# Performance work log

Hardware: AMD Instinct MI355X
Metric: run time of the kernel (lower is better)

Reference implementation:

```python
import jax, jax.numpy as jnp
import numpy as np

B, P, K = 32, 2048, 20   # events, points per event, kNN neighbors
EPS = 1e-5               # BatchNorm eps (eval mode, running stats)


def setup_inputs() -> dict:
    key = jax.random.key(0)
    ks = iter(jax.random.split(key, 64))
    inp = {}
    inp["x"] = jax.random.normal(next(ks), (B * P, 7), jnp.float32)
    inp["batch"] = jnp.repeat(jnp.arange(B, dtype=jnp.int32), P)

    def add_layer(tag, cin, cout):
        inp["w" + tag] = jax.random.normal(next(ks), (cin, cout), jnp.float32) / np.sqrt(cin)
        inp["b" + tag] = jax.random.normal(next(ks), (cout,), jnp.float32) * 0.01
        inp["g" + tag] = jax.random.uniform(next(ks), (cout,), jnp.float32, 0.5, 1.5)
        inp["e" + tag] = jax.random.normal(next(ks), (cout,), jnp.float32) * 0.1
        inp["m" + tag] = jax.random.normal(next(ks), (cout,), jnp.float32) * 0.1
        inp["v" + tag] = jax.random.uniform(next(ks), (cout,), jnp.float32, 0.5, 1.5)

    # conv1 MLP: [14, 64, 64, 64]
    add_layer("10", 14, 64)
    add_layer("11", 64, 64)
    add_layer("12", 64, 64)
    # conv2 MLP: [128, 128]
    add_layer("20", 128, 128)
    return inp


def _lin_relu_bn(h, W, b, g, be, rm, rv):
    # Linear -> ReLU -> BatchNorm1d (eval mode: running stats)
    h = jax.nn.relu(h @ W + b)
    return (h - rm) * (g / jnp.sqrt(rv + EPS)) + be


def _knn_idx(x):
    # x: [B, P, C] -> indices of K nearest neighbors (incl. self), [B, P, K]
    sq = jnp.sum(x * x, axis=-1)                                   # [B, P]
    d = sq[:, :, None] + sq[:, None, :] - 2.0 * jnp.einsum("bpc,bqc->bpq", x, x)
    _, idx = jax.lax.top_k(-d, K)
    return idx


def _edge_conv(x, mlp):
    # DynamicEdgeConv: kNN graph on current features, edge MLP([x_i, x_j - x_i]), max-aggr
    idx = _knn_idx(x)                                              # [B, P, K]
    xj = jax.vmap(lambda xb, ib: xb[ib])(x, idx)                   # [B, P, K, C]
    xi = jnp.broadcast_to(x[:, :, None, :], xj.shape)
    e = jnp.concatenate([xi, xj - xi], axis=-1)                    # [B, P, K, 2C]
    return jnp.max(mlp(e), axis=2)                                 # [B, P, Cout]


def reference(x, batch,
              w10, b10, g10, e10, m10, v10,
              w11, b11, g11, e11, m11, v11,
              w12, b12, g12, e12, m12, v12,
              w20, b20, g20, e20, m20, v20):
    xb = x.reshape(B, P, -1)                                       # fixed-size events

    def mlp1(e):
        h = _lin_relu_bn(e, w10, b10, g10, e10, m10, v10)
        h = _lin_relu_bn(h, w11, b11, g11, e11, m11, v11)
        return _lin_relu_bn(h, w12, b12, g12, e12, m12, v12)

    def mlp2(e):
        return _lin_relu_bn(e, w20, b20, g20, e20, m20, v20)

    x1 = _edge_conv(xb, mlp1)                                      # [B, P, 64]
    x2 = _edge_conv(x1, mlp2)                                      # [B, P, 128]
    out = jnp.concatenate([x1, x2], axis=-1).reshape(B * P, 192)
    return out, batch
```

## Files before the change

### kernel.cpp

```cpp
#include <hip/hip_runtime.h>

#define B_EV 32
#define P_PT 2048
#define K_NN 20
#define NPTS (B_EV*P_PT)
#define EPS_BN 1e-5f
#define RINF 3.0e38f

typedef _Float16 half8 __attribute__((ext_vector_type(8)));
typedef float f32x4 __attribute__((ext_vector_type(4)));

static constexpr int oWA10=0, oWB10=448, oB10=896, oT10=960,
  oT11=5184,
  oT12=9408,
  oWA20=9472, oWB20=17664, oB20=25856, oT20=25984,
  oB11p=26048, oB12p=26112,
  oW11hi=26176, oW11lo=28224,
  oW12hi=30272, oW12lo=32320;
static constexpr size_t oIDX = 36864;
static constexpr size_t oA1  = 1347584;
static constexpr size_t oB1  = oA1 + (size_t)NPTS*64;
static constexpr size_t oV2  = oB1 + (size_t)NPTS*64;
static constexpr size_t oX1  = oV2 + (size_t)NPTS*128;
static constexpr size_t oSQ  = oX1 + (size_t)NPTS*64;
static constexpr size_t oU2  = oA1;

__global__ __launch_bounds__(128) void k_prep(
  const float* w10,const float* b10,const float* g10,const float* e10,const float* m10,const float* v10,
  const float* w11,const float* b11,const float* g11,const float* e11,const float* m11,const float* v11,
  const float* w12,const float* b12,const float* g12,const float* e12,const float* m12,const float* v12,
  const float* w20,const float* b20,const float* g20,const float* e20,const float* m20,const float* v20,
  float* ws)
{
  __shared__ float t10s[64], t11s[64];
  int c = threadIdx.x;
  if (c < 64) {
    float s0 = g10[c]*rsqrtf(v10[c]+EPS_BN);
    ws[oB10+c]=b10[c]*s0;
    float t10 = e10[c]-m10[c]*s0; ws[oT10+c]=t10; t10s[c]=t10;
    for (int i=0;i<7;i++){
      ws[oWA10+i*64+c]=(w10[i*64+c]-w10[(7+i)*64+c])*s0;
      ws[oWB10+i*64+c]=w10[(7+i)*64+c]*s0;
    }
    float s1 = g11[c]*rsqrtf(v11[c]+EPS_BN);
    float t11 = e11[c]-m11[c]*s1; ws[oT11+c]=t11; t11s[c]=t11;
    float s2 = g12[c]*rsqrtf(v12[c]+EPS_BN);
    ws[oT12+c]=e12[c]-m12[c]*s2;
  }
  __syncthreads();
  if (c < 64) {
    float s1 = g11[c]*rsqrtf(v11[c]+EPS_BN);
    _Float16* W1hi = (_Float16*)(ws + oW11hi);
    _Float16* W1lo = (_Float16*)(ws + oW11lo);
    float acc = b11[c]*s1;
    for (int i=0;i<64;i++){
      float wv = w11[i*64+c]*s1;
      _Float16 h = (_Float16)wv;
      W1hi[c*64+i] = h;
      W1lo[c*64+i] = (_Float16)(wv - (float)h);
      acc = fmaf(t10s[i], wv, acc);
    }
    ws[oB11p+c]=acc;
    float s2 = g12[c]*rsqrtf(v12[c]+EPS_BN);
    _Float16* W2hi = (_Float16*)(ws + oW12hi);
    _Float16* W2lo = (_Float16*)(ws + oW12lo);
    float acc2 = b12[c]*s2;
    for (int i=0;i<64;i++){
      float wv = w12[i*64+c]*s2;
      _Float16 h = (_Float16)wv;
      W2hi[c*64+i] = h;
      W2lo[c*64+i] = (_Float16)(wv - (float)h);
      acc2 = fmaf(t11s[i], wv, acc2);
    }
    ws[oB12p+c]=acc2;
  }
  {
    float s = g20[c]*rsqrtf(v20[c]+EPS_BN);
    ws[oB20+c]=b20[c]*s; ws[oT20+c]=e20[c]-m20[c]*s;
    for (int i=0;i<64;i++){
      ws[oWA20+i*128+c]=(w20[i*128+c]-w20[(64+i)*128+c])*s;
      ws[oWB20+i*128+c]=w20[(64+i)*128+c]*s;
    }
  }
}

__device__ __forceinline__ void select20(float (&d)[32], int lane, int base, int g,
                                         int* __restrict__ idxout)
{
  float g4[4];
  #pragma unroll
  for (int k=0;k<4;k++){
    float m = d[8*k];
    #pragma unroll
    for (int j=1;j<8;j++) m = fminf(m, d[8*k+j]);
    g4[k]=m;
  }
  float T = 0.f;
  #pragma unroll 1
  for (int pass=0; pass<20; ++pass){
    float m = fminf(fminf(g4[0],g4[1]), fminf(g4[2],g4[3]));
    #pragma unroll
    for (int off=32; off>0; off>>=1) m = fminf(m, __shfl_xor(m, off, 64));
    if (pass==19){ T=m; break; }
    #pragma unroll
    for (int k=0;k<4;k++){
      if (g4[k]==m){
        #pragma unroll
        for (int j=0;j<8;j++) d[8*k+j] = (d[8*k+j]==m) ? RINF : d[8*k+j];
        float mm = d[8*k];
        #pragma unroll
        for (int j=1;j<8;j++) mm = fminf(mm, d[8*k+j]);
        g4[k]=mm;
      }
    }
  }
  int cnt=0;
  #pragma unroll
  for (int j=0;j<32;j++){
    bool take = (d[j]>=RINF) || (d[j]==T);
    unsigned long long mb = __ballot(take);
    if (take){
      int pos = cnt + (int)__popcll(mb & ((1ull<<lane)-1ull));
      if (pos < K_NN) idxout[(size_t)g*K_NN + pos] = base + j*64 + lane;
    }
    cnt += (int)__popcll(mb);
  }
  if (lane==0){
    for (int r=cnt; r<K_NN; ++r) idxout[(size_t)g*K_NN + r] = g;
  }
}

__global__ __launch_bounds__(1024, 8) void k_knn1(const float* __restrict__ x, int* __restrict__ idxout)
{
  __shared__ float xs[P_PT*8];
  int t = threadIdx.x;
  int b = blockIdx.x;
  int xcd = b & 7, kk = b >> 3;
  int e = xcd + ((kk >> 7) << 3);
  int blk = kk & 127;
  {
    const float* xe = x + (size_t)e*P_PT*7;
    #pragma unroll
    for (int u=0; u<2; u++){
      int p = t + u*1024;
      float v0=xe[p*7+0], v1=xe[p*7+1], v2=xe[p*7+2], v3=xe[p*7+3];
      float v4=xe[p*7+4], v5=xe[p*7+5], v6=xe[p*7+6];
      int s = (p&7)<<2;
      int w0 = (p*8) ^ s;
      int w1 = (p*8+4) ^ s;
      f32x4 lo = {v0,v1,v2,v3};
      f32x4 hi = {v4,v5,v6,0.f};
      *(f32x4*)(xs + w0) = lo;
      *(f32x4*)(xs + w1) = hi;
    }
  }
  __syncthreads();
  int lane = t & 63;
  int g = e*P_PT + blk*16 + (t>>6);
  int pin = g & (P_PT-1);
  float xp[7];
  {
    int s = (pin&7)<<2;
    f32x4 lo = *(const f32x4*)(xs + ((pin*8)^s));
    f32x4 hi = *(const f32x4*)(xs + ((pin*8+4)^s));
    xp[0]=lo[0]; xp[1]=lo[1]; xp[2]=lo[2]; xp[3]=lo[3];
    xp[4]=hi[0]; xp[5]=hi[1]; xp[6]=hi[2];
  }
  int sl = (lane&7)<<2;
  const float* base0 = xs + ((lane*8)^sl);
  const float* base1 = xs + ((lane*8+4)^sl);
  float d[32];
  #pragma unroll
  for (int j=0;j<32;j++){
    f32x4 lo = *(const f32x4*)(base0 + j*512);
    f32x4 hi = *(const f32x4*)(base1 + j*512);
    float s=0.f, df;
    df = xp[0]-lo[0]; s=fmaf(df,df,s);
    df = xp[1]-lo[1]; s=fmaf(df,df,s);
    df = xp[2]-lo[2]; s=fmaf(df,df,s);
    df = xp[3]-lo[3]; s=fmaf(df,df,s);
    df = xp[4]-hi[0]; s=fmaf(df,df,s);
    df = xp[5]-hi[1]; s=fmaf(df,df,s);
    df = xp[6]-hi[2]; s=fmaf(df,df,s);
    d[j]=s;
  }
  select20(d, lane, e*P_PT, g, idxout);
}

__global__ __launch_bounds__(256) void k_ab1(const float* __restrict__ x, const float* __restrict__ W,
                                             float* __restrict__ A1, float* __restrict__ B1)
{
  int g = blockIdx.x*256+threadIdx.x;
  float xi[7];
  #pragma unroll
  for (int i=0;i<7;i++) xi[i]=x[(size_t)g*7+i];
  float a[64], b[64];
  #pragma unroll
  for (int c=0;c<64;c++){ a[c]=W[oB10+c]; b[c]=0.f; }
  #pragma unroll
  for (int i=0;i<7;i++){
    #pragma unroll
    for (int c=0;c<64;c++) a[c]=fmaf(xi[i], W[oWA10+i*64+c], a[c]);
    #pragma unroll
    for (int c=0;c<64;c++) b[c]=fmaf(xi[i], W[oWB10+i*64+c], b[c]);
  }
  #pragma unroll
  for (int c=0;c<64;c+=4){
    float4 oa; oa.x=a[c]; oa.y=a[c+1]; oa.z=a[c+2]; oa.w=a[c+3];
    *(float4*)(A1+(size_t)g*64+c)=oa;
    float4 ob; ob.x=b[c]; ob.y=b[c+1]; ob.z=b[c+2]; ob.w=b[c+3];
    *(float4*)(B1+(size_t)g*64+c)=ob;
  }
}

__global__ __launch_bounds__(256, 2) void k_ec1m(const int* __restrict__ idx, const float* __restrict__ ws,
    const float* __restrict__ A1, const float* __restrict__ B1,
    float* __restrict__ x1, float* __restrict__ sqv, float* __restrict__ out)
{
  __shared__ float h2s[4][48*64];
  int t = threadIdx.x, w = t>>6, lane = t&63;
  int b = blockIdx.x;
  int xcd = b & 7, kk = b >> 3;
  int ev = xcd + ((kk >> 8) << 3);
  int iA = ev*P_PT + (kk & 255)*8 + w*2;
  int iB = iA + 1;
  int lg = lane>>4, lr = lane&15;

  int jT0 = idx[(size_t)iA*K_NN + lr];
  int jT1 = idx[(size_t)iB*K_NN + lr];
  int a2 = (lr < 4) ? iA*K_NN + 16 + lr : iB*K_NN + 12 + lr;
  a2 = (lr < 8) ? a2 : 0;
  int jT2 = (lr < 8) ? idx[a2] : iA;

  const float* ApA = A1 + (size_t)iA*64;
  const float* ApB = A1 + (size_t)iB*64;
  float4 avA[2][2], avB[2][2], bv[3][2][2];
  const float* Bp0 = B1 + (size_t)jT0*64;
  const float* Bp1 = B1 + (size_t)jT1*64;
  const float* Bp2 = B1 + (size_t)jT2*64;
  #pragma unroll
  for (int ks=0;ks<2;ks++){
    int c0 = ks*32 + lg*8;
    avA[ks][0] = *(const float4*)(ApA+c0); avA[ks][1] = *(const float4*)(ApA+c0+4);
    avB[ks][0] = *(const float4*)(ApB+c0); avB[ks][1] = *(const float4*)(ApB+c0+4);
    bv[0][ks][0] = *(const float4*)(Bp0+c0); bv[0][ks][1] = *(const float4*)(Bp0+c0+4);
    bv[1][ks][0] = *(const float4*)(Bp1+c0); bv[1][ks][1] = *(const float4*)(Bp1+c0+4);
    bv[2][ks][0] = *(const float4*)(Bp2+c0); bv[2][ks][1] = *(const float4*)(Bp2+c0+4);
  }

  bool useB2 = (lr >= 4) && (lr < 8);
  half8 AH[3][2], AL[3][2];
  #pragma unroll
  for (int tile=0;tile<3;tile++){
    #pragma unroll
    for (int ks=0;ks<2;ks++){
      float4 a0, a1;
      if (tile==0){ a0 = avA[ks][0]; a1 = avA[ks][1]; }
      else if (tile==1){ a0 = avB[ks][0]; a1 = avB[ks][1]; }
      else {
        a0.x = useB2 ? avB[ks][0].x : avA[ks][0].x;  a0.y = useB2 ? avB[ks][0].y : avA[ks][0].y;
        a0.z = useB2 ? avB[ks][0].z : avA[ks][0].z;  a0.w = useB2 ? avB[ks][0].w : avA[ks][0].w;
        a1.x = useB2 ? avB[ks][1].x : avA[ks][1].x;  a1.y = useB2 ? avB[ks][1].y : avA[ks][1].y;
        a1.z = useB2 ? avB[ks][1].z : avA[ks][1].z;  a1.w = useB2 ? avB[ks][1].w : avA[ks][1].w;
      }
      float hv[8];
      hv[0]=fmaxf(a0.x+bv[tile][ks][0].x,0.f); hv[1]=fmaxf(a0.y+bv[tile][ks][0].y,0.f);
      hv[2]=fmaxf(a0.z+bv[tile][ks][0].z,0.f); hv[3]=fmaxf(a0.w+bv[tile][ks][0].w,0.f);
      hv[4]=fmaxf(a1.x+bv[tile][ks][1].x,0.f); hv[5]=fmaxf(a1.y+bv[tile][ks][1].y,0.f);
      hv[6]=fmaxf(a1.z+bv[tile][ks][1].z,0.f); hv[7]=fmaxf(a1.w+bv[tile][ks][1].w,0.f);
      half8 ah, al;
      #pragma unroll
      for (int q=0;q<8;q++){
        _Float16 h = (_Float16)hv[q];
        ah[q]=h; al[q]=(_Float16)(hv[q]-(float)h);
      }
      AH[tile][ks]=ah; AL[tile][ks]=al;
    }
  }

  f32x4 acc[3][4];
  #pragma unroll
  for (int nt=0;nt<4;nt++){
    float bb = ws[oB11p + nt*16 + lr];
    f32x4 v = {bb,bb,bb,bb};
    acc[0][nt]=v; acc[1][nt]=v; acc[2][nt]=v;
  }
  {
    const _Float16* W1hi = (const _Float16*)(ws + oW11hi);
    const _Float16* W1lo = (const _Float16*)(ws + oW11lo);
    #pragma unroll
    for (int nt=0;nt<4;nt++){
      const _Float16* whp = W1hi + (nt*16+lr)*64 + lg*8;
      const _Float16* wlp = W1lo + (nt*16+lr)*64 + lg*8;
      half8 wh0 = *(const half8*)(whp);
      half8 wh1 = *(const half8*)(whp+32);
      half8 wl0 = *(const half8*)(wlp);
      half8 wl1 = *(const half8*)(wlp+32);
      #pragma unroll
      for (int tile=0;tile<3;tile++){
        acc[tile][nt] = __builtin_amdgcn_mfma_f32_16x16x32_f16(AH[tile][0], wh0, acc[tile][nt], 0,0,0);
        acc[tile][nt] = __builtin_amdgcn_mfma_f32_16x16x32_f16(AL[tile][0], wh0, acc[tile][nt], 0,0,0);
        acc[tile][nt] = __builtin_amdgcn_mfma_f32_16x16x32_f16(AH[tile][0], wl0, acc[tile][nt], 0,0,0);
        acc[tile][nt] = __builtin_amdgcn_mfma_f32_16x16x32_f16(AH[tile][1], wh1, acc[tile][nt], 0,0,0);
        acc[tile][nt] = __builtin_amdgcn_mfma_f32_16x16x32_f16(AL[tile][1], wh1, acc[tile][nt], 0,0,0);
        acc[tile][nt] = __builtin_amdgcn_mfma_f32_16x16x32_f16(AH[tile][1], wl1, acc[tile][nt], 0,0,0);
      }
    }
  }

  float* hb = h2s[w];
  #pragma unroll
  for (int tile=0;tile<3;tile++){
    #pragma unroll
    for (int nt=0;nt<4;nt++){
      #pragma unroll
      for (int r=0;r<4;r++){
        int row = tile*16 + lg*4 + r;
        int col = nt*16 + lr;
        int baddr = (row*256 + col*4) ^ ((row&7)<<4);
        *(float*)((char*)hb + baddr) = fmaxf(acc[tile][nt][r], 0.f);
      }
    }
  }

  half8 AH2[3][2], AL2[3][2];
  #pragma unroll
  for (int tile=0;tile<3;tile++){
    #pragma unroll
    for (int ks=0;ks<2;ks++){
      int row = tile*16 + lr;
      int byte0 = (row*256 + (ks*32 + lg*8)*4);
      int s = (row&7)<<4;
      f32x4 v0 = *(const f32x4*)((char*)hb + ((byte0)^s));
      f32x4 v1 = *(const f32x4*)((char*)hb + ((byte0+16)^s));
      half8 ah, al;
      #pragma unroll
      for (int q=0;q<4;q++){
        _Float16 h = (_Float16)v0[q];
        ah[q]=h; al[q]=(_Float16)(v0[q]-(float)h);
      }
      #pragma unroll
      for (int q=0;q<4;q++){
        _Float16 h = (_Float16)v1[q];
        ah[4+q]=h; al[4+q]=(_Float16)(v1[q]-(float)h);
      }
      AH2[tile][ks]=ah; AL2[tile][ks]=al;
    }
  }

  f32x4 acc2[3][4];
  #pragma unroll
  for (int nt=0;nt<4;nt++){
    float bb = ws[oB12p + nt*16 + lr];
    f32x4 v = {bb,bb,bb,bb};
    acc2[0][nt]=v; acc2[1][nt]=v; acc2[2][nt]=v;
  }
  {
    const _Float16* W2hi = (const _Float16*)(ws + oW12hi);
    const _Float16* W2lo = (const _Float16*)(ws + oW12lo);
    #pragma unroll
    for (int nt=0;nt<4;nt++){
      const _Float16* whp = W2hi + (nt*16+lr)*64 + lg*8;
      const _Float16* wlp = W2lo + (nt*16+lr)*64 + lg*8;
      half8 wh0 = *(const half8*)(whp);
      half8 wh1 = *(const half8*)(whp+32);
      half8 wl0 = *(const half8*)(wlp);
      half8 wl1 = *(const half8*)(wlp+32);
      #pragma unroll
      for (int tile=0;tile<3;tile++){
        acc2[tile][nt] = __builtin_amdgcn_mfma_f32_16x16x32_f16(AH2[tile][0], wh0, acc2[tile][nt], 0,0,0);
        acc2[tile][nt] = __builtin_amdgcn_mfma_f32_16x16x32_f16(AL2[tile][0], wh0, acc2[tile][nt], 0,0,0);
        acc2[tile][nt] = __builtin_amdgcn_mfma_f32_16x16x32_f16(AH2[tile][0], wl0, acc2[tile][nt], 0,0,0);
        acc2[tile][nt] = __builtin_amdgcn_mfma_f32_16x16x32_f16(AH2[tile][1], wh1, acc2[tile][nt], 0,0,0);
        acc2[tile][nt] = __builtin_amdgcn_mfma_f32_16x16x32_f16(AL2[tile][1], wh1, acc2[tile][nt], 0,0,0);
        acc2[tile][nt] = __builtin_amdgcn_mfma_f32_16x16x32_f16(AH2[tile][1], wl1, acc2[tile][nt], 0,0,0);
      }
    }
  }

  float finA[4], finB[4];
  float sqA = 0.f, sqB = 0.f;
  #pragma unroll
  for (int nt=0;nt<4;nt++){
    float cvA = -RINF;
    #pragma unroll
    for (int r=0;r<4;r++) cvA = fmaxf(cvA, acc2[0][nt][r]);
    if (lg==0){
      #pragma unroll
      for (int r=0;r<4;r++) cvA = fmaxf(cvA, acc2[2][nt][r]);
    }
    cvA = fmaxf(cvA, __shfl_xor(cvA,16,64));
    cvA = fmaxf(cvA, __shfl_xor(cvA,32,64));
    finA[nt] = fmaxf(cvA, 0.f) + ws[oT12 + nt*16 + lr];
    sqA = fmaf(finA[nt], finA[nt], sqA);

    float cvB = -RINF;
    #pragma unroll
    for (int r=0;r<4;r++) cvB = fmaxf(cvB, acc2[1][nt][r]);
    if (lg==1){
      #pragma unroll
      for (int r=0;r<4;r++) cvB = fmaxf(cvB, acc2[2][nt][r]);
    }
    cvB = fmaxf(cvB, __shfl_xor(cvB,16,64));
    cvB = fmaxf(cvB, __shfl_xor(cvB,32,64));
    finB[nt] = fmaxf(cvB, 0.f) + ws[oT12 + nt*16 + lr];
    sqB = fmaf(finB[nt], finB[nt], sqB);
  }
  if (lane < 16){
    #pragma unroll
    for (int nt=0;nt<4;nt++){
      x1[(size_t)iA*64 + nt*16 + lane] = finA[nt];
      out[(size_t)iA*192 + nt*16 + lane] = finA[nt];
      x1[(size_t)iB*64 + nt*16 + lane] = finB[nt];
      out[(size_t)iB*192 + nt*16 + lane] = finB[nt];
    }
  }
  #pragma unroll
  for (int off=1; off<16; off<<=1){
    sqA += __shfl_xor(sqA, off, 64);
    sqB += __shfl_xor(sqB, off, 64);
  }
  if (lane == 0){ sqv[iA] = sqA; sqv[iB] = sqB; }
}

__global__ __launch_bounds__(1024, 4) void k_dsel(const float* __restrict__ x1,
    const float* __restrict__ sqv, int* __restrict__ idxout)
{
  __shared__ float cs[16][260];
  int t = threadIdx.x, w = t>>6, lane = t&63;
  int b = blockIdx.x;
  int xcd = b & 7, kk = b >> 3;
  int e = xcd + ((kk >> 7) << 3);
  int base16 = e*P_PT + (kk & 127)*16;
  int lg = lane>>4, lr = lane&15;

  half8 AH[2], AL[2];
  {
    const float* Ap = x1 + (size_t)(base16 + lr)*64;
    #pragma unroll
    for (int kx=0;kx<2;kx++){
      float4 a0 = *(const float4*)(Ap + kx*32 + lg*8);
      float4 a1 = *(const float4*)(Ap + kx*32 + lg*8 + 4);
      float hv[8] = {a0.x,a0.y,a0.z,a0.w,a1.x,a1.y,a1.z,a1.w};
      half8 ah, al;
      #pragma unroll
      for (int q=0;q<8;q++){
        _Float16 h = (_Float16)hv[q];
        ah[q]=h; al[q]=(_Float16)(hv[q]-(float)h);
      }
      AH[kx]=ah; AL[kx]=al;
    }
  }
  int p = base16 + w;
  float sqp = sqv[p];
  const float* Xe = x1 + (size_t)e*P_PT*64;
  const float* sqe = sqv + e*P_PT;

  float d[32];
  #pragma unroll 1
  for (int chunk=0; chunk<8; ++chunk){
    int c = chunk*256 + w*16 + lr;
    const float* Bp = Xe + (size_t)c*64;
    f32x4 acc = {0.f,0.f,0.f,0.f};
    #pragma unroll
    for (int kx=0;kx<2;kx++){
      float4 b0 = *(const float4*)(Bp + kx*32 + lg*8);
      float4 b1 = *(const float4*)(Bp + kx*32 + lg*8 + 4);
      float hv[8] = {b0.x,b0.y,b0.z,b0.w,b1.x,b1.y,b1.z,b1.w};
      half8 bh, bl;
      #pragma unroll
      for (int q=0;q<8;q++){
        _Float16 h = (_Float16)hv[q];
        bh[q]=h; bl[q]=(_Float16)(hv[q]-(float)h);
      }
      acc = __builtin_amdgcn_mfma_f32_16x16x32_f16(AH[kx], bh, acc, 0,0,0);
      acc = __builtin_amdgcn_mfma_f32_16x16x32_f16(AL[kx], bh, acc, 0,0,0);
      acc = __builtin_amdgcn_mfma_f32_16x16x32_f16(AH[kx], bl, acc, 0,0,0);
      acc = __builtin_amdgcn_mfma_f32_16x16x32_f16(AL[kx], bl, acc, 0,0,0);
    }
    #pragma unroll
    for (int r=0;r<4;r++) cs[4*lg + r][w*16 + lr] = acc[r];
    __syncthreads();
    #pragma unroll
    for (int jj=0;jj<4;jj++){
      float sqc = sqe[chunk*256 + jj*64 + lane];
      d[chunk*4 + jj] = sqp + sqc - 2.f*cs[w][jj*64 + lane];
    }
    __syncthreads();
  }
  select20(d, lane, e*P_PT, p, idxout);
}

__global__ __launch_bounds__(256) void k_uv2(const float* __restrict__ x1, const float* __restrict__ W,
                                             float* __restrict__ U2, float* __restrict__ V2)
{
  int g = blockIdx.x*256 + threadIdx.x;
  int half = blockIdx.y & 1;
  bool isU = blockIdx.y < 2;
  const float* Wb = W + (isU?oWA20:oWB20) + half*64;
  float acc[64];
  #pragma unroll
  for (int c=0;c<64;c++) acc[c] = isU ? W[oB20+half*64+c] : 0.f;
  const float* xp = x1 + (size_t)g*64;
  #pragma unroll 1
  for (int i=0;i<64;i+=4){
    float4 xv = *(const float4*)(xp+i);
    #pragma unroll
    for (int c=0;c<64;c++) acc[c]=fmaf(xv.x, Wb[(i+0)*128+c], acc[c]);
    #pragma unroll
    for (int c=0;c<64;c++) acc[c]=fmaf(xv.y, Wb[(i+1)*128+c], acc[c]);
    #pragma unroll
    for (int c=0;c<64;c++) acc[c]=fmaf(xv.z, Wb[(i+2)*128+c], acc[c]);
    #pragma unroll
    for (int c=0;c<64;c++) acc[c]=fmaf(xv.w, Wb[(i+3)*128+c], acc[c]);
  }
  float* dst = (isU?U2:V2) + (size_t)g*128 + half*64;
  #pragma unroll
  for (int c=0;c<64;c+=4){
    float4 o; o.x=acc[c]; o.y=acc[c+1]; o.z=acc[c+2]; o.w=acc[c+3];
    *(float4*)(dst+c)=o;
  }
}

__global__ __launch_bounds__(256) void k_gather2(const int* __restrict__ idx, const float* __restrict__ U2,
     const float* __restrict__ V2, const float* __restrict__ W, const int* __restrict__ batch,
     float* __restrict__ out)
{
  int b = blockIdx.x;
  int xcd = b & 7, kk = b >> 3;
  int ev = xcd + ((kk >> 3) << 3);
  int g = ev*P_PT + (kk & 7)*256 + threadIdx.x;
  int half = blockIdx.y;
  if (half == 0) out[(size_t)NPTS*192 + g] = (float)batch[g];
  float mx[64];
  #pragma unroll
  for (int c=0;c<64;c++) mx[c]=-RINF;
  for (int k=0;k<K_NN;k++){
    int j = idx[(size_t)g*K_NN+k];
    const float4* vp = (const float4*)(V2 + (size_t)j*128 + half*64);
    #pragma unroll
    for (int c4=0;c4<16;c4++){
      float4 v=vp[c4];
      mx[c4*4+0]=fmaxf(mx[c4*4+0],v.x);
      mx[c4*4+1]=fmaxf(mx[c4*4+1],v.y);
      mx[c4*4+2]=fmaxf(mx[c4*4+2],v.z);
      mx[c4*4+3]=fmaxf(mx[c4*4+3],v.w);
    }
  }
  const float* Up = U2 + (size_t)g*128 + half*64;
  float* op = out + (size_t)g*192 + 64 + half*64;
  #pragma unroll
  for (int c=0;c<64;c+=4){
    float4 o;
    o.x = fmaxf(Up[c+0]+mx[c+0],0.f)+W[oT20+half*64+c+0];
    o.y = fmaxf(Up[c+1]+mx[c+1],0.f)+W[oT20+half*64+c+1];
    o.z = fmaxf(Up[c+2]+mx[c+2],0.f)+W[oT20+half*64+c+2];
    o.w = fmaxf(Up[c+3]+mx[c+3],0.f)+W[oT20+half*64+c+3];
    *(float4*)(op+c)=o;
  }
}

extern "C" void kernel_launch(void* const* d_in, const int* in_sizes, int n_in,
                              void* d_out, int out_size, void* d_ws, size_t ws_size,
                              hipStream_t stream)
{
  const float* x     = (const float*)d_in[0];
  const int*   batch = (const int*)d_in[1];
  const float* w10=(const float*)d_in[2],  *b10=(const float*)d_in[3],  *g10=(const float*)d_in[4],
             *e10=(const float*)d_in[5],  *m10=(const float*)d_in[6],  *v10=(const float*)d_in[7];
  const float* w11=(const float*)d_in[8],  *b11=(const float*)d_in[9],  *g11=(const float*)d_in[10],
             *e11=(const float*)d_in[11], *m11=(const float*)d_in[12], *v11=(const float*)d_in[13];
  const float* w12=(const float*)d_in[14], *b12=(const float*)d_in[15], *g12=(const float*)d_in[16],
             *e12=(const float*)d_in[17], *m12=(const float*)d_in[18], *v12=(const float*)d_in[19];
  const float* w20=(const float*)d_in[20], *b20=(const float*)d_in[21], *g20=(const float*)d_in[22],
             *e20=(const float*)d_in[23], *m20=(const float*)d_in[24], *v20=(const float*)d_in[25];

  float* ws  = (float*)d_ws;
  float* out = (float*)d_out;
  int*   idxp = (int*)(ws + oIDX);

  k_prep<<<1,128,0,stream>>>(w10,b10,g10,e10,m10,v10, w11,b11,g11,e11,m11,v11,
                             w12,b12,g12,e12,m12,v12, w20,b20,g20,e20,m20,v20, ws);
  k_knn1<<<NPTS/16, 1024, 0, stream>>>(x, idxp);
  k_ab1<<<NPTS/256, 256, 0, stream>>>(x, ws, ws+oA1, ws+oB1);
  k_ec1m<<<NPTS/8, 256, 0, stream>>>(idxp, ws, ws+oA1, ws+oB1, ws+oX1, ws+oSQ, out);
  k_dsel<<<NPTS/16, 1024, 0, stream>>>(ws+oX1, ws+oSQ, idxp);
  k_uv2<<<dim3(NPTS/256,4),256,0,stream>>>(ws+oX1, ws, ws+oU2, ws+oV2);
  k_gather2<<<dim3(NPTS/256,2),256,0,stream>>>(idxp, ws+oU2, ws+oV2, ws, batch, out);
}
```

Measured before the change: 1.096 ms.

## Precompute fp16 hi/lo split of x1 in edge-conv kernel; halve dsel barriers

The edge-conv kernel now writes x1 a second time as two fp16 arrays, a high part and a residual low part, so the distance/select kernel loads half8 operands directly. This removes the fp32 loads and per-element conversion in the MFMA distance loop. The dsel loop also processes 512 candidates per shared-memory round instead of 256, which halves the number of __syncthreads and doubles the LDS buffer. The cost is extra global writes in k_ec1m, plus more shared memory per block, which could reduce occupancy.

```diff
diff --git a/kernel.cpp b/kernel.cpp
--- a/kernel.cpp
+++ b/kernel.cpp
@@ -23,6 +23,8 @@
 static constexpr size_t oV2  = oB1 + (size_t)NPTS*64;
 static constexpr size_t oX1  = oV2 + (size_t)NPTS*128;
 static constexpr size_t oSQ  = oX1 + (size_t)NPTS*64;
+static constexpr size_t oX1H = oSQ + (size_t)NPTS;
+static constexpr size_t oX1L = oX1H + (size_t)NPTS*32;
 static constexpr size_t oU2  = oA1;
 
 __global__ __launch_bounds__(128) void k_prep(
@@ -215,7 +217,8 @@
 
 __global__ __launch_bounds__(256, 2) void k_ec1m(const int* __restrict__ idx, const float* __restrict__ ws,
     const float* __restrict__ A1, const float* __restrict__ B1,
-    float* __restrict__ x1, float* __restrict__ sqv, float* __restrict__ out)
+    float* __restrict__ x1, _Float16* __restrict__ x1h, _Float16* __restrict__ x1l,
+    float* __restrict__ sqv, float* __restrict__ out)
 {
   __shared__ float h2s[4][48*64];
   int t = threadIdx.x, w = t>>6, lane = t&63;
@@ -413,6 +416,12 @@
       out[(size_t)iA*192 + nt*16 + lane] = finA[nt];
       x1[(size_t)iB*64 + nt*16 + lane] = finB[nt];
       out[(size_t)iB*192 + nt*16 + lane] = finB[nt];
+      _Float16 hA = (_Float16)finA[nt];
+      x1h[(size_t)iA*64 + nt*16 + lane] = hA;
+      x1l[(size_t)iA*64 + nt*16 + lane] = (_Float16)(finA[nt]-(float)hA);
+      _Float16 hB = (_Float16)finB[nt];
+      x1h[(size_t)iB*64 + nt*16 + lane] = hB;
+      x1l[(size_t)iB*64 + nt*16 + lane] = (_Float16)(finB[nt]-(float)hB);
     }
   }
   #pragma unroll
@@ -423,10 +432,10 @@
   if (lane == 0){ sqv[iA] = sqA; sqv[iB] = sqB; }
 }
 
-__global__ __launch_bounds__(1024, 4) void k_dsel(const float* __restrict__ x1,
-    const float* __restrict__ sqv, int* __restrict__ idxout)
-{
-  __shared__ float cs[16][260];
+__global__ __launch_bounds__(1024, 4) void k_dsel(const _Float16* __restrict__ x1h,
+    const _Float16* __restrict__ x1l, const float* __restrict__ sqv, int* __restrict__ idxout)
+{
+  __shared__ float cs[16][520];
   int t = threadIdx.x, w = t>>6, lane = t&63;
   int b = blockIdx.x;
   int xcd = b & 7, kk = b >> 3;
@@ -436,55 +445,46 @@
 
   half8 AH[2], AL[2];
   {
-    const float* Ap = x1 + (size_t)(base16 + lr)*64;
+    const _Float16* Ah = x1h + (size_t)(base16 + lr)*64;
+    const _Float16* Al = x1l + (size_t)(base16 + lr)*64;
     #pragma unroll
     for (int kx=0;kx<2;kx++){
-      float4 a0 = *(const float4*)(Ap + kx*32 + lg*8);
-      float4 a1 = *(const float4*)(Ap + kx*32 + lg*8 + 4);
-      float hv[8] = {a0.x,a0.y,a0.z,a0.w,a1.x,a1.y,a1.z,a1.w};
-      half8 ah, al;
-      #pragma unroll
-      for (int q=0;q<8;q++){
-        _Float16 h = (_Float16)hv[q];
-        ah[q]=h; al[q]=(_Float16)(hv[q]-(float)h);
-      }
-      AH[kx]=ah; AL[kx]=al;
+      AH[kx] = *(const half8*)(Ah + kx*32 + lg*8);
+      AL[kx] = *(const half8*)(Al + kx*32 + lg*8);
     }
   }
   int p = base16 + w;
   float sqp = sqv[p];
-  const float* Xe = x1 + (size_t)e*P_PT*64;
+  const _Float16* Xh = x1h + (size_t)e*P_PT*64;
+  const _Float16* Xl = x1l + (size_t)e*P_PT*64;
   const float* sqe = sqv + e*P_PT;
 
   float d[32];
   #pragma unroll 1
-  for (int chunk=0; chunk<8; ++chunk){
-    int c = chunk*256 + w*16 + lr;
-    const float* Bp = Xe + (size_t)c*64;
-    f32x4 acc = {0.f,0.f,0.f,0.f};
-    #pragma unroll
-    for (int kx=0;kx<2;kx++){
-      float4 b0 = *(const float4*)(Bp + kx*32 + lg*8);
-      float4 b1 = *(const float4*)(Bp + kx*32 + lg*8 + 4);
-      float hv[8] = {b0.x,b0.y,b0.z,b0.w,b1.x,b1.y,b1.z,b1.w};
-      half8 bh, bl;
-      #pragma unroll
-      for (int q=0;q<8;q++){
-        _Float16 h = (_Float16)hv[q];
-        bh[q]=h; bl[q]=(_Float16)(hv[q]-(float)h);
-      }
-      acc = __builtin_amdgcn_mfma_f32_16x16x32_f16(AH[kx], bh, acc, 0,0,0);
-      acc = __builtin_amdgcn_mfma_f32_16x16x32_f16(AL[kx], bh, acc, 0,0,0);
-      acc = __builtin_amdgcn_mfma_f32_16x16x32_f16(AH[kx], bl, acc, 0,0,0);
-      acc = __builtin_amdgcn_mfma_f32_16x16x32_f16(AL[kx], bl, acc, 0,0,0);
-    }
-    #pragma unroll
-    for (int r=0;r<4;r++) cs[4*lg + r][w*16 + lr] = acc[r];
+  for (int cc=0; cc<4; ++cc){
+    #pragma unroll
+    for (int hh=0; hh<2; hh++){
+      int c = cc*512 + hh*256 + w*16 + lr;
+      const _Float16* Bh = Xh + (size_t)c*64;
+      const _Float16* Bl = Xl + (size_t)c*64;
+      f32x4 acc = {0.f,0.f,0.f,0.f};
+      #pragma unroll
+      for (int kx=0;kx<2;kx++){
+        half8 bh = *(const half8*)(Bh + kx*32 + lg*8);
+        half8 bl = *(const half8*)(Bl + kx*32 + lg*8);
+        acc = __builtin_amdgcn_mfma_f32_16x16x32_f16(AH[kx], bh, acc, 0,0,0);
+        acc = __builtin_amdgcn_mfma_f32_16x16x32_f16(AL[kx], bh, acc, 0,0,0);
+        acc = __builtin_amdgcn_mfma_f32_16x16x32_f16(AH[kx], bl, acc, 0,0,0);
+        acc = __builtin_amdgcn_mfma_f32_16x16x32_f16(AL[kx], bl, acc, 0,0,0);
+      }
+      #pragma unroll
+      for (int r=0;r<4;r++) cs[4*lg + r][hh*256 + w*16 + lr] = acc[r];
+    }
     __syncthreads();
     #pragma unroll
-    for (int jj=0;jj<4;jj++){
-      float sqc = sqe[chunk*256 + jj*64 + lane];
-      d[chunk*4 + jj] = sqp + sqc - 2.f*cs[w][jj*64 + lane];
+    for (int jj=0;jj<8;jj++){
+      float sqc = sqe[cc*512 + jj*64 + lane];
+      d[cc*8 + jj] = sqp + sqc - 2.f*cs[w][jj*64 + lane];
     }
     __syncthreads();
   }
@@ -578,13 +578,15 @@
   float* ws  = (float*)d_ws;
   float* out = (float*)d_out;
   int*   idxp = (int*)(ws + oIDX);
+  _Float16* x1h = (_Float16*)(ws + oX1H);
+  _Float16* x1l = (_Float16*)(ws + oX1L);
 
   k_prep<<<1,128,0,stream>>>(w10,b10,g10,e10,m10,v10, w11,b11,g11,e11,m11,v11,
                              w12,b12,g12,e12,m12,v12, w20,b20,g20,e20,m20,v20, ws);
   k_knn1<<<NPTS/16, 1024, 0, stream>>>(x, idxp);
   k_ab1<<<NPTS/256, 256, 0, stream>>>(x, ws, ws+oA1, ws+oB1);
-  k_ec1m<<<NPTS/8, 256, 0, stream>>>(idxp, ws, ws+oA1, ws+oB1, ws+oX1, ws+oSQ, out);
-  k_dsel<<<NPTS/16, 1024, 0, stream>>>(ws+oX1, ws+oSQ, idxp);
+  k_ec1m<<<NPTS/8, 256, 0, stream>>>(idxp, ws, ws+oA1, ws+oB1, ws+oX1, x1h, x1l, ws+oSQ, out);
+  k_dsel<<<NPTS/16, 1024, 0, stream>>>(x1h, x1l, ws+oSQ, idxp);
   k_uv2<<<dim3(NPTS/256,4),256,0,stream>>>(ws+oX1, ws, ws+oU2, ws+oV2);
   k_gather2<<<dim3(NPTS/256,2),256,0,stream>>>(idxp, ws+oU2, ws+oV2, ws, batch, out);
 }
```

Result: faster. 1.057 ms (-3.5%).
